# Kernel tuning notes

Measured on AMD Instinct MI355X. Metric: run time of the kernel, lower is better.

The kernel has to match this reference:

```python
import jax, jax.numpy as jnp
import numpy as np

N = 50000
LEAKY_SLOPE = 0.2


def gat_layer(x, src, dst, W, a_src, a_dst, bias, concat):
    """PyG-style GATConv (eval mode, self-loops already in src/dst).
    x: [N, Fin]; W: [Fin, H*C]; a_src, a_dst: [H, C]; bias: [H*C] or [C].
    """
    H, C = a_src.shape
    h = (x @ W).reshape(-1, H, C)                      # [N, H, C]
    alpha_src = jnp.einsum('nhc,hc->nh', h, a_src)      # [N, H]
    alpha_dst = jnp.einsum('nhc,hc->nh', h, a_dst)      # [N, H]
    e = jax.nn.leaky_relu(alpha_src[src] + alpha_dst[dst], LEAKY_SLOPE)  # [E, H]
    # scatter-softmax over incoming edges of each destination node
    m = jax.lax.stop_gradient(jax.ops.segment_max(e, dst, num_segments=N))
    e = jnp.exp(e - m[dst])
    denom = jax.ops.segment_sum(e, dst, num_segments=N)  # [N, H]
    alpha = e / (denom[dst] + 1e-16)                     # [E, H]
    msg = h[src] * alpha[:, :, None]                     # [E, H, C]
    out = jax.ops.segment_sum(msg, dst, num_segments=N)  # [N, H, C]
    out = out.reshape(-1, H * C) if concat else out.mean(axis=1)
    return out + bias


def setup_inputs() -> dict:
    key = jax.random.key(0)
    ks = jax.random.split(key, 10)
    Fin, Hd, Hh = 256, 64, 4
    E = 1600000
    x = jax.random.normal(ks[0], (N, Fin), dtype=jnp.float32)
    edge_index = jax.random.randint(ks[1], (2, E), 0, N, dtype=jnp.int64)
    s = 1.0 / np.sqrt(Fin)
    W1 = jax.random.normal(ks[2], (Fin, Hh * Hd), dtype=jnp.float32) * s
    att_src1 = jax.random.normal(ks[3], (Hh, Hd), dtype=jnp.float32) * (1.0 / np.sqrt(Hd))
    att_dst1 = jax.random.normal(ks[4], (Hh, Hd), dtype=jnp.float32) * (1.0 / np.sqrt(Hd))
    b1 = jnp.zeros((Hh * Hd,), dtype=jnp.float32)
    W2 = jax.random.normal(ks[5], (Hh * Hd, Hd), dtype=jnp.float32) * (1.0 / np.sqrt(Hh * Hd))
    att_src2 = jax.random.normal(ks[6], (1, Hd), dtype=jnp.float32) * (1.0 / np.sqrt(Hd))
    att_dst2 = jax.random.normal(ks[7], (1, Hd), dtype=jnp.float32) * (1.0 / np.sqrt(Hd))
    b2 = jnp.zeros((Hd,), dtype=jnp.float32)
    return {"x": x, "edge_index": edge_index, "W1": W1, "att_src1": att_src1,
            "att_dst1": att_dst1, "b1": b1, "W2": W2, "att_src2": att_src2,
            "att_dst2": att_dst2, "b2": b2}


def reference(x, edge_index, W1, att_src1, att_dst1, b1, W2, att_src2, att_dst2, b2):
    # PyG GATConv adds self-loops by default
    loop = jnp.arange(N, dtype=edge_index.dtype)
    src = jnp.concatenate([edge_index[0], loop])
    dst = jnp.concatenate([edge_index[1], loop])
    h = gat_layer(x, src, dst, W1, att_src1, att_dst1, b1, concat=True)
    h = jax.nn.elu(h)            # dropout is identity in eval mode
    out = gat_layer(h, src, dst, W2, att_src2, att_dst2, b2, concat=False)
    return out
```

## Files before the change

kernel.cpp:

```cpp
#include <hip/hip_runtime.h>


typedef __attribute__((ext_vector_type(8))) short short8;
typedef __attribute__((ext_vector_type(4))) float floatx4;
typedef __attribute__((ext_vector_type(2))) float fx2;
typedef __attribute__((ext_vector_type(4))) unsigned int uintx4;

#define FIN 256
#define H1 4
#define CH 64
#define CAP 16384
#define G2S 40

__device__ __forceinline__ float bf2f(ushort u) {
    union { unsigned int i; float f; } v; v.i = ((unsigned int)u) << 16; return v.f;
}
__device__ __forceinline__ ushort f2bf(float f) {
    union { float f; unsigned int i; } v; v.f = f;
    unsigned int r = v.i + 0x7fffu + ((v.i >> 16) & 1u);
    return (ushort)(r >> 16);
}
__device__ __forceinline__ float load_in(const void* p, int i, int f) {
    return f ? ((const float*)p)[i] : bf2f(((const ushort*)p)[i]);
}
__device__ __forceinline__ int load_idx(const void* p, long long i, int f64) {
    return f64 ? (int)((const long long*)p)[i] : ((const int*)p)[i];
}

__device__ __forceinline__ int pk_off(int row, int k, int KT) {
    return (((row >> 4) * KT + (k >> 5)) << 9) + (((k >> 3) & 3) << 7) +
           ((row & 15) << 3) + (k & 7);
}
__device__ __forceinline__ void pk_dec(int po0, int& row, int& k) {
    int tile = po0 >> 9;
    row = ((tile >> 3) << 4) + ((po0 >> 3) & 15);
    k = ((tile & 7) << 5) + (((po0 >> 7) & 3) << 3);
}

__device__ __forceinline__ float edge_p(float s) {
    s = fmaxf(s, 0.2f * s);
    return __expf(s);
}

__device__ __forceinline__ void accum16(fx2* acc, uint4 v0, uint4 v1,
                                        float p, float& l) {
    l += p;
    fx2 pv = {p, p};
    unsigned w[8] = {v0.x, v0.y, v0.z, v0.w, v1.x, v1.y, v1.z, v1.w};
#pragma unroll
    for (int u = 0; u < 8; ++u) {
        union { unsigned i; float fl; } lo, hi;
        lo.i = w[u] << 16; hi.i = w[u] & 0xffff0000u;
        fx2 c = {lo.fl, hi.fl};
        acc[u] += pv * c;
    }
}

__device__ __forceinline__ void accum8(fx2* acc, uint4 v, float p, float& l) {
    l += p;
    fx2 pv = {p, p};
    unsigned w[4] = {v.x, v.y, v.z, v.w};
#pragma unroll
    for (int u = 0; u < 4; ++u) {
        union { unsigned i; float fl; } lo, hi;
        lo.i = w[u] << 16; hi.i = w[u] & 0xffff0000u;
        fx2 c = {lo.fl, hi.fl};
        acc[u] += pv * c;
    }
}

__global__ __launch_bounds__(256) void probe_kernel(const ushort* __restrict__ x,
                                                    const int* __restrict__ ei,
                                                    int* __restrict__ flags,
                                                    int* __restrict__ bcnt) {
    __shared__ int s_nan, s_odd;
    int t = threadIdx.x;
    bcnt[t] = 0;
    if (t == 0) { s_nan = 0; s_odd = 0; }
    __syncthreads();
    int nanc = 0, oddc = 0;
    for (int i = t; i < 16384; i += 256) {
        ushort u = x[i];
        if (((u >> 7) & 0xFF) == 0xFF) nanc++;
    }
    for (int i = t; i < 2048; i += 256)
        if (ei[2 * i + 1] != 0) oddc++;
    if (nanc) atomicAdd(&s_nan, nanc);
    if (oddc) atomicAdd(&s_odd, oddc);
    __syncthreads();
    if (t == 0) {
        flags[0] = (s_nan >= 2) ? 1 : 0;
        flags[1] = (s_odd == 0) ? 1 : 0;
    }
}

__global__ __launch_bounds__(256) void prep_bucket_kernel(
        const void* __restrict__ x, const void* __restrict__ W1,
        const void* __restrict__ W2, ushort* __restrict__ xb,
        ushort* __restrict__ Wt1, ushort* __restrict__ Wt2,
        const void* __restrict__ ei, int* __restrict__ bcnt,
        unsigned int* __restrict__ buckets,
        int E, int Etot, int Nn, const int* __restrict__ flags,
        int PB_conv, int PB_tr_end) {
    __shared__ int lcnt[256], lbase[256], lcur[256];
    int bid = blockIdx.x, t = threadIdx.x;
    int f = flags[0];
    if (bid < PB_conv) {
        int po0 = bid * 2048 + t * 8;
        int row, k0; pk_dec(po0, row, k0);
        int si = row * FIN + k0;
        if (f) {
            float4 v0 = ((const float4*)x)[si / 4];
            float4 v1 = ((const float4*)x)[si / 4 + 1];
            ushort4 o0, o1;
            o0.x = f2bf(v0.x); o0.y = f2bf(v0.y); o0.z = f2bf(v0.z); o0.w = f2bf(v0.w);
            o1.x = f2bf(v1.x); o1.y = f2bf(v1.y); o1.z = f2bf(v1.z); o1.w = f2bf(v1.w);
            *(ushort4*)(xb + po0) = o0;
            *(ushort4*)(xb + po0 + 4) = o1;
        } else {
            *(uint4*)(xb + po0) = ((const uint4*)x)[si / 8];
        }
        return;
    }
    if (bid < PB_tr_end) {
        int j = (bid - PB_conv) * 256 + t;
        if (j < (FIN * FIN) / 8) {
            int po0 = j * 8;
            int n, k0; pk_dec(po0, n, k0);
            ushort4 o0, o1;
            o0.x = f2bf(load_in(W1, (k0 + 0) * FIN + n, f));
            o0.y = f2bf(load_in(W1, (k0 + 1) * FIN + n, f));
            o0.z = f2bf(load_in(W1, (k0 + 2) * FIN + n, f));
            o0.w = f2bf(load_in(W1, (k0 + 3) * FIN + n, f));
            o1.x = f2bf(load_in(W1, (k0 + 4) * FIN + n, f));
            o1.y = f2bf(load_in(W1, (k0 + 5) * FIN + n, f));
            o1.z = f2bf(load_in(W1, (k0 + 6) * FIN + n, f));
            o1.w = f2bf(load_in(W1, (k0 + 7) * FIN + n, f));
            *(ushort4*)(Wt1 + po0) = o0;
            *(ushort4*)(Wt1 + po0 + 4) = o1;
        } else {
            int po0 = (j - (FIN * FIN) / 8) * 8;
            int n, k0; pk_dec(po0, n, k0);
            ushort4 o0, o1;
            o0.x = f2bf(load_in(W2, (k0 + 0) * CH + n, f));
            o0.y = f2bf(load_in(W2, (k0 + 1) * CH + n, f));
            o0.z = f2bf(load_in(W2, (k0 + 2) * CH + n, f));
            o0.w = f2bf(load_in(W2, (k0 + 3) * CH + n, f));
            o1.x = f2bf(load_in(W2, (k0 + 4) * CH + n, f));
            o1.y = f2bf(load_in(W2, (k0 + 5) * CH + n, f));
            o1.z = f2bf(load_in(W2, (k0 + 6) * CH + n, f));
            o1.w = f2bf(load_in(W2, (k0 + 7) * CH + n, f));
            *(ushort4*)(Wt2 + po0) = o0;
            *(ushort4*)(Wt2 + po0 + 4) = o1;
        }
        return;
    }
    lcnt[t] = 0; lcur[t] = 0;
    __syncthreads();
    int f64 = flags[1];
    int base = (bid - PB_tr_end) * 4096 + t;
    unsigned int val[16]; int bk[16]; bool ok[16];
#pragma unroll
    for (int j = 0; j < 16; ++j) {
        int e = base + j * 256;
        ok[j] = e < Etot;
        bk[j] = 0; val[j] = 0;
        if (ok[j]) {
            int s, d;
            if (e < E) {
                s = load_idx(ei, e, f64);
                d = load_idx(ei, (long long)E + e, f64);
            } else {
                s = d = e - E;
            }
            s = min(max(s, 0), Nn - 1);
            d = min(max(d, 0), Nn - 1);
            bk[j] = d >> 8;
            val[j] = ((unsigned int)s << 8) | (unsigned int)(d & 255);
            atomicAdd(&lcnt[bk[j]], 1);
        }
    }
    __syncthreads();
    if (lcnt[t] > 0) lbase[t] = atomicAdd(&bcnt[t], lcnt[t]);
    __syncthreads();
#pragma unroll
    for (int j = 0; j < 16; ++j) {
        if (ok[j]) {
            int p = lbase[bk[j]] + atomicAdd(&lcur[bk[j]], 1);
            if (p < CAP) buckets[(size_t)bk[j] * CAP + p] = val[j];
        }
    }
}

__device__ __forceinline__ void gemm_core(const ushort* __restrict__ A,
                                          const ushort* __restrict__ Bt,
                                          ushort* __restrict__ C,
                                          int M,
                                          const void* __restrict__ aS,
                                          const void* __restrict__ aD,
                                          float* __restrict__ alphaS,
                                          float* __restrict__ alphaD,
                                          int f, int gx, int head) {
    const int KT = FIN >> 5;
    int tid = threadIdx.x;
    int wave = tid >> 6, lane = tid & 63, quad = lane >> 4, l16 = lane & 15;
    int rbase = gx * 256 + wave * 64;
    int cbase = head * 64;
    int lsub = (quad << 7) + (l16 << 3);
    floatx4 acc[4][4];
#pragma unroll
    for (int i = 0; i < 4; i++)
#pragma unroll
        for (int j = 0; j < 4; j++) acc[i][j] = (floatx4)0.f;

#pragma unroll 2
    for (int kb = 0; kb < FIN; kb += 32) {
        int kt = kb >> 5;
        short8 a[4], b[4];
#pragma unroll
        for (int mt = 0; mt < 4; mt++) {
            int tr = (rbase + mt * 16) >> 4;
            a[mt] = *reinterpret_cast<const short8*>(
                A + (((size_t)(tr * KT + kt)) << 9) + lsub);
        }
#pragma unroll
        for (int nt = 0; nt < 4; nt++) {
            int tc = (cbase + nt * 16) >> 4;
            b[nt] = *reinterpret_cast<const short8*>(
                Bt + (((size_t)(tc * KT + kt)) << 9) + lsub);
        }
#pragma unroll
        for (int mt = 0; mt < 4; mt++)
#pragma unroll
            for (int nt = 0; nt < 4; nt++)
                acc[mt][nt] = __builtin_amdgcn_mfma_f32_16x16x32_bf16(
                    a[mt], b[nt], acc[mt][nt], 0, 0, 0);
    }
    float asv[4], adv[4];
#pragma unroll
    for (int nt = 0; nt < 4; nt++) {
        int col = cbase + nt * 16 + l16;
        asv[nt] = load_in(aS, col, f);
        adv[nt] = load_in(aD, col, f);
    }
#pragma unroll
    for (int mt = 0; mt < 4; mt++) {
#pragma unroll
        for (int r = 0; r < 4; r++) {
            int row = rbase + mt * 16 + quad * 4 + r;
            float ps = 0.f, pd = 0.f;
#pragma unroll
            for (int nt = 0; nt < 4; nt++) {
                float w = acc[mt][nt][r];
                ps += w * asv[nt];
                pd += w * adv[nt];
            }
#pragma unroll
            for (int off = 8; off > 0; off >>= 1) {
                ps += __shfl_xor(ps, off, 16);
                pd += __shfl_xor(pd, off, 16);
            }
            if (row < M) {
                if (l16 == 0) {
                    alphaS[row * H1 + head] = ps;
                    alphaD[row * H1 + head] = pd;
                }
#pragma unroll
                for (int nt = 0; nt < 4; nt++) {
                    int col = cbase + nt * 16 + l16;
                    size_t caddr = ((size_t)(col >> 7) * M + row) * 128 + (col & 127);
                    C[caddr] = f2bf(acc[mt][nt][r]);
                }
            }
        }
    }
}

__global__ __launch_bounds__(256) void gemm1_pass2_kernel(
        const ushort* __restrict__ A, const ushort* __restrict__ Bt,
        ushort* __restrict__ C, int M,
        const void* __restrict__ aS, const void* __restrict__ aD,
        float* __restrict__ alphaS, float* __restrict__ alphaD,
        const int* __restrict__ flags, int NB, int nbx,
        const int* __restrict__ bcnt, const unsigned int* __restrict__ buckets,
        int* __restrict__ offs, int* __restrict__ csr_src, int Nn) {
    __shared__ int part[256], sc[256], sc4[4][256];
    int bid = blockIdx.x;
    int t = threadIdx.x;
    if (bid >= NB) {
        int gg = bid - NB;
        int r = (gg & 7) | ((gg >> 5) << 3);
        int h = (gg >> 3) & 3;
        if (r < nbx)
            gemm_core(A, Bt, C, M, aS, aD, alphaS, alphaD, flags[0], r, h);
        return;
    }
    int b = bid;
    int w = t >> 6;
    part[t] = bcnt[t];
    sc4[0][t] = 0; sc4[1][t] = 0; sc4[2][t] = 0; sc4[3][t] = 0;
    __syncthreads();
#pragma unroll
    for (int off = 1; off < 256; off <<= 1) {
        int v = (t >= off) ? part[t - off] : 0;
        __syncthreads();
        part[t] += v;
        __syncthreads();
    }
    int basepos = (b == 0) ? 0 : part[b - 1];
    int nEdges = min(bcnt[b], CAP);
    const unsigned int* bk = buckets + (size_t)b * CAP;
    for (int i = t; i < nEdges; i += 256)
        atomicAdd(&sc4[w][bk[i] & 255], 1);
    __syncthreads();
    int c0 = sc4[0][t], c1 = sc4[1][t], c2 = sc4[2][t], c3 = sc4[3][t];
    int mycount = c0 + c1 + c2 + c3;
    sc[t] = mycount;
    __syncthreads();
#pragma unroll
    for (int off = 1; off < 256; off <<= 1) {
        int v = (t >= off) ? sc[t - off] : 0;
        __syncthreads();
        sc[t] += v;
        __syncthreads();
    }
    int excl = sc[t] - mycount;
    int gnode = b * 256 + t;
    if (gnode <= Nn) offs[gnode] = basepos + excl;
    sc4[0][t] = excl;
    sc4[1][t] = excl + c0;
    sc4[2][t] = excl + c0 + c1;
    sc4[3][t] = excl + c0 + c1 + c2;
    __syncthreads();
    for (int i = t; i < nEdges; i += 256) {
        unsigned int v = bk[i];
        int p = atomicAdd(&sc4[w][v & 255], 1);
        csr_src[basepos + p] = (int)(v >> 8);
    }
}

__global__ __launch_bounds__(256) void gemm2_kernel(const ushort* __restrict__ A,
                                                    const ushort* __restrict__ Bt,
                                                    ushort* __restrict__ C,
                                                    int M,
                                                    const void* __restrict__ aS,
                                                    const void* __restrict__ aD,
                                                    float* __restrict__ alphaS,
                                                    float* __restrict__ alphaD,
                                                    const int* __restrict__ flags) {
    __shared__ ushort Asub[256 * G2S];
    const int KT = FIN >> 5;
    int t = threadIdx.x;
    int f = flags[0];
    int wave = t >> 6, lane = t & 63, quad = lane >> 4, l16 = lane & 15;
    int rbase = blockIdx.x * 256 + wave * 64;
    int lsub = (quad << 7) + (l16 << 3);
    int chunk = t & 3, rr = t >> 2;
    floatx4 acc[4][4];
#pragma unroll
    for (int i = 0; i < 4; i++)
#pragma unroll
        for (int j = 0; j < 4; j++) acc[i][j] = (floatx4)0.f;

    for (int kb = 0; kb < FIN; kb += 32) {
        __syncthreads();
#pragma unroll
        for (int rd = 0; rd < 4; ++rd) {
            int row = blockIdx.x * 256 + rd * 64 + rr;
            if (row >= M) row = M - 1;
            uint4 v = *(const uint4*)(A + (size_t)row * FIN + kb + chunk * 8);
            *(uint4*)(Asub + (rd * 64 + rr) * G2S + chunk * 8) = v;
        }
        __syncthreads();
        int kt = kb >> 5;
        short8 b[4];
#pragma unroll
        for (int nt = 0; nt < 4; nt++) {
            b[nt] = *reinterpret_cast<const short8*>(
                Bt + (((size_t)(nt * KT + kt)) << 9) + lsub);
        }
#pragma unroll
        for (int mt = 0; mt < 4; mt++) {
            short8 a = *reinterpret_cast<const short8*>(
                Asub + (wave * 64 + mt * 16 + l16) * G2S + quad * 8);
#pragma unroll
            for (int nt = 0; nt < 4; nt++)
                acc[mt][nt] = __builtin_amdgcn_mfma_f32_16x16x32_bf16(
                    a, b[nt], acc[mt][nt], 0, 0, 0);
        }
    }
    float asv[4], adv[4];
#pragma unroll
    for (int nt = 0; nt < 4; nt++) {
        int col = nt * 16 + l16;
        asv[nt] = load_in(aS, col, f);
        adv[nt] = load_in(aD, col, f);
    }
#pragma unroll
    for (int mt = 0; mt < 4; mt++) {
#pragma unroll
        for (int r = 0; r < 4; r++) {
            int row = rbase + mt * 16 + quad * 4 + r;
            float ps = 0.f, pd = 0.f;
#pragma unroll
            for (int nt = 0; nt < 4; nt++) {
                float w = acc[mt][nt][r];
                ps += w * asv[nt];
                pd += w * adv[nt];
            }
#pragma unroll
            for (int off = 8; off > 0; off >>= 1) {
                ps += __shfl_xor(ps, off, 16);
                pd += __shfl_xor(pd, off, 16);
            }
            if (row < M) {
                if (l16 == 0) {
                    alphaS[row] = ps;
                    alphaD[row] = pd;
                }
#pragma unroll
                for (int nt = 0; nt < 4; nt++) {
                    int col = nt * 16 + l16;
                    C[(size_t)row * CH + col] = f2bf(acc[mt][nt][r]);
                }
            }
        }
    }
}

__global__ __launch_bounds__(256) void gat_node1_pass(
        const int* __restrict__ csr_src, const int* __restrict__ offs,
        const float* __restrict__ asrc, const float* __restrict__ adst,
        const ushort* __restrict__ h1p, const void* __restrict__ b1,
        ushort* __restrict__ hmidb, int Nn, const int* __restrict__ flags,
        int plane) {
    int f = flags[0];
    int wave = threadIdx.x >> 6, lane = threadIdx.x & 63;
    int n = blockIdx.x * 4 + wave;
    if (n >= Nn) return;
    int slot = lane >> 3, cg = lane & 7;
    int head = plane * 2 + (cg >> 2);
    float ad = adst[n * H1 + head];
    unsigned rowbase = (unsigned)(plane * Nn) * 128u + (unsigned)cg * 16u;
    int beg = offs[n], end = offs[n + 1];
    fx2 acc[8];
#pragma unroll
    for (int u = 0; u < 8; ++u) acc[u] = (fx2)0.f;
    float l = 0.f;

    int e = beg;
    while (e + 16 <= end) {
        int sa = csr_src[e + slot];
        int sb = csr_src[e + 8 + slot];
        float aa = asrc[sa * H1 + head];
        float ab = asrc[sb * H1 + head];
        const uint4* ra = (const uint4*)(h1p + rowbase + (unsigned)sa * 128u);
        const uint4* rb = (const uint4*)(h1p + rowbase + (unsigned)sb * 128u);
        uint4 va0 = ra[0], va1 = ra[1];
        uint4 vb0 = rb[0], vb1 = rb[1];
        float pa = edge_p(aa + ad);
        float pb = edge_p(ab + ad);
        accum16(acc, va0, va1, pa, l);
        accum16(acc, vb0, vb1, pb, l);
        e += 16;
    }
    if (e < end) {
        int ea = e + slot, eb = e + 8 + slot;
        bool oka = ea < end, okb = eb < end;
        int sa = csr_src[oka ? ea : beg];
        int sb = csr_src[okb ? eb : beg];
        float aa = asrc[sa * H1 + head];
        float ab = asrc[sb * H1 + head];
        const uint4* ra = (const uint4*)(h1p + rowbase + (unsigned)sa * 128u);
        const uint4* rb = (const uint4*)(h1p + rowbase + (unsigned)sb * 128u);
        uint4 va0 = ra[0], va1 = ra[1];
        uint4 vb0 = rb[0], vb1 = rb[1];
        float pa = edge_p(oka ? aa + ad : -1e30f);
        float pb = edge_p(okb ? ab + ad : -1e30f);
        accum16(acc, va0, va1, pa, l);
        accum16(acc, vb0, vb1, pb, l);
    }
#pragma unroll
    for (int off = 8; off <= 32; off <<= 1) {
#pragma unroll
        for (int u = 0; u < 8; ++u) {
            acc[u][0] += __shfl_xor(acc[u][0], off);
            acc[u][1] += __shfl_xor(acc[u][1], off);
        }
        l += __shfl_xor(l, off);
    }
    if (slot == 0) {
        float inv = 1.f / (l + 1e-16f);
        int cb = plane * 128 + cg * 16;
        unsigned ow[8];
#pragma unroll
        for (int u = 0; u < 8; ++u) {
            float o0 = acc[u][0] * inv + load_in(b1, cb + 2 * u, f);
            float o1 = acc[u][1] * inv + load_in(b1, cb + 2 * u + 1, f);
            o0 = o0 > 0.f ? o0 : __expf(o0) - 1.f;
            o1 = o1 > 0.f ? o1 : __expf(o1) - 1.f;
            ow[u] = (unsigned)f2bf(o0) | ((unsigned)f2bf(o1) << 16);
        }
        uintx4 st0 = {ow[0], ow[1], ow[2], ow[3]};
        uintx4 st1 = {ow[4], ow[5], ow[6], ow[7]};
        uintx4* dst = (uintx4*)(hmidb + (size_t)n * 256 + cb);
        __builtin_nontemporal_store(st0, dst);
        __builtin_nontemporal_store(st1, dst + 1);
    }
}

__global__ __launch_bounds__(256) void gat_node2(const int* __restrict__ csr_src,
                                                 const int* __restrict__ offs,
                                                 const float* __restrict__ asrc,
                                                 const float* __restrict__ adst,
                                                 const ushort* __restrict__ h2b,
                                                 const void* __restrict__ b2,
                                                 void* __restrict__ out, int Nn,
                                                 const int* __restrict__ flags) {
    int f = flags[0];
    int wave = threadIdx.x >> 6, lane = threadIdx.x & 63;
    int n = blockIdx.x * 4 + wave;
    if (n >= Nn) return;
    int slot = lane >> 3, cg = lane & 7;
    float ad = adst[n];
    unsigned rowoff = (unsigned)cg * 8u;
    int beg = offs[n], end = offs[n + 1];
    fx2 acc[4];
#pragma unroll
    for (int u = 0; u < 4; ++u) acc[u] = (fx2)0.f;
    float l = 0.f;

    int e = beg;
    while (e + 16 <= end) {
        int sa = csr_src[e + slot];
        int sb = csr_src[e + 8 + slot];
        float aa = asrc[sa];
        float ab = asrc[sb];
        uint4 va = *(const uint4*)(h2b + rowoff + (unsigned)sa * 64u);
        uint4 vb = *(const uint4*)(h2b + rowoff + (unsigned)sb * 64u);
        float pa = edge_p(aa + ad);
        float pb = edge_p(ab + ad);
        accum8(acc, va, pa, l);
        accum8(acc, vb, pb, l);
        e += 16;
    }
    if (e < end) {
        int ea = e + slot, eb = e + 8 + slot;
        bool oka = ea < end, okb = eb < end;
        int sa = csr_src[oka ? ea : beg];
        int sb = csr_src[okb ? eb : beg];
        float aa = asrc[sa];
        float ab = asrc[sb];
        uint4 va = *(const uint4*)(h2b + rowoff + (unsigned)sa * 64u);
        uint4 vb = *(const uint4*)(h2b + rowoff + (unsigned)sb * 64u);
        float pa = edge_p(oka ? aa + ad : -1e30f);
        float pb = edge_p(okb ? ab + ad : -1e30f);
        accum8(acc, va, pa, l);
        accum8(acc, vb, pb, l);
    }
#pragma unroll
    for (int off = 8; off <= 32; off <<= 1) {
#pragma unroll
        for (int u = 0; u < 4; ++u) {
            acc[u][0] += __shfl_xor(acc[u][0], off);
            acc[u][1] += __shfl_xor(acc[u][1], off);
        }
        l += __shfl_xor(l, off);
    }
    if (slot == 0) {
        float inv = 1.f / (l + 1e-16f);
        float o[8];
#pragma unroll
        for (int u = 0; u < 4; ++u) {
            o[2 * u]     = acc[u][0] * inv + load_in(b2, cg * 8 + 2 * u, f);
            o[2 * u + 1] = acc[u][1] * inv + load_in(b2, cg * 8 + 2 * u + 1, f);
        }
        if (f) {
            float* op = (float*)out + (unsigned)n * 64u + (unsigned)cg * 8u;
            floatx4 s0 = {o[0], o[1], o[2], o[3]};
            floatx4 s1 = {o[4], o[5], o[6], o[7]};
            __builtin_nontemporal_store(s0, (floatx4*)op);
            __builtin_nontemporal_store(s1, (floatx4*)(op + 4));
        } else {
            uintx4 st = {(unsigned)f2bf(o[0]) | ((unsigned)f2bf(o[1]) << 16),
                         (unsigned)f2bf(o[2]) | ((unsigned)f2bf(o[3]) << 16),
                         (unsigned)f2bf(o[4]) | ((unsigned)f2bf(o[5]) << 16),
                         (unsigned)f2bf(o[6]) | ((unsigned)f2bf(o[7]) << 16)};
            __builtin_nontemporal_store(st,
                (uintx4*)((ushort*)out + (unsigned)n * 64u + (unsigned)cg * 8u));
        }
    }
}

extern "C" void kernel_launch(void* const* d_in, const int* in_sizes, int n_in,
                              void* d_out, int out_size, void* d_ws, size_t ws_size,
                              hipStream_t stream) {
    const void* x   = d_in[0];
    const void* ei  = d_in[1];
    const void* W1  = d_in[2];
    const void* as1 = d_in[3];
    const void* ad1 = d_in[4];
    const void* b1  = d_in[5];
    const void* W2  = d_in[6];
    const void* as2 = d_in[7];
    const void* ad2 = d_in[8];
    const void* b2  = d_in[9];

    const int Nn = in_sizes[0] / FIN;
    const int E  = in_sizes[1] / 2;
    const int ET = E + Nn;
    const int NB = (Nn + 255) >> 8;

    char* ws = (char*)d_ws;
    size_t off = 0;
    auto alloc = [&](size_t bytes) {
        size_t o = off;
        off += (bytes + 255) & ~(size_t)255;
        return o;
    };
    ushort* xb    = (ushort*)(ws + alloc((size_t)Nn * FIN * 2));
    ushort* h1b   = (ushort*)(ws + alloc((size_t)Nn * FIN * 2));
    ushort* hmidb = (ushort*)(ws + alloc((size_t)Nn * FIN * 2));
    ushort* h2b   = (ushort*)(ws + alloc((size_t)Nn * CH * 2));
    ushort* Wt1   = (ushort*)(ws + alloc((size_t)FIN * FIN * 2));
    ushort* Wt2   = (ushort*)(ws + alloc((size_t)CH * FIN * 2));
    float* as1f   = (float*)(ws + alloc((size_t)Nn * H1 * 4));
    float* ad1f   = (float*)(ws + alloc((size_t)Nn * H1 * 4));
    float* as2f   = (float*)(ws + alloc((size_t)Nn * 4));
    float* ad2f   = (float*)(ws + alloc((size_t)Nn * 4));
    int*   offs   = (int*)(ws + alloc((size_t)(Nn + 1) * 4));
    int*   csr    = (int*)(ws + alloc((size_t)ET * 4));
    unsigned int* buckets = (unsigned int*)(ws + alloc((size_t)256 * CAP * 4));
    int*   bcnt   = (int*)(ws + alloc(256 * 4));
    int*   flags  = (int*)(ws + alloc(256));
    (void)ws_size; (void)n_in; (void)out_size;

    probe_kernel<<<1, 256, 0, stream>>>((const ushort*)x, (const int*)ei, flags, bcnt);

    int PB_conv = (Nn * FIN) / 2048;
    int PB_tr   = (FIN * FIN + CH * FIN) / 2048;
    int PB_bkt  = (ET + 4095) / 4096;
    prep_bucket_kernel<<<PB_conv + PB_tr + PB_bkt, 256, 0, stream>>>(
        x, W1, W2, xb, Wt1, Wt2, ei, bcnt, buckets,
        E, ET, Nn, flags, PB_conv, PB_conv + PB_tr);

    int nbx = (Nn + 255) / 256;
    int ngrp = (nbx + 7) >> 3;
    gemm1_pass2_kernel<<<NB + ngrp * 32, 256, 0, stream>>>(
        xb, Wt1, h1b, Nn, as1, ad1, as1f, ad1f,
        flags, NB, nbx, bcnt, buckets, offs, csr, Nn);

    gat_node1_pass<<<(Nn + 3) / 4, 256, 0, stream>>>(
        csr, offs, as1f, ad1f, h1b, b1, hmidb, Nn, flags, 0);
    gat_node1_pass<<<(Nn + 3) / 4, 256, 0, stream>>>(
        csr, offs, as1f, ad1f, h1b, b1, hmidb, Nn, flags, 1);

    gemm2_kernel<<<(Nn + 255) / 256, 256, 0, stream>>>(
        hmidb, Wt2, h2b, Nn, as2, ad2, as2f, ad2f, flags);
    gat_node2<<<(Nn + 3) / 4, 256, 0, stream>>>(csr, offs, as2f, ad2f, h2b, b2, d_out, Nn, flags);
}
```

Measured before the change: 344.8 us.

## Read raw bf16 input directly in GEMM1 via LDS staging, skip packing copy

When the input is already bf16, the prep kernel no longer repacks x into the MFMA-tiled layout. GEMM1 instead stages row-major tiles of raw x into a padded shared-memory buffer and feeds MFMA from LDS. This removes a full pass over the input array, at the cost of two block barriers per K step and extra LDS in the fused kernel, which may lower occupancy for the bucket/CSR blocks. The probe kernel is also vectorised to uint4 loads.

```diff
diff --git a/kernel.cpp b/kernel.cpp
--- a/kernel.cpp
+++ b/kernel.cpp
@@ -69,8 +69,8 @@
     }
 }
 
-__global__ __launch_bounds__(256) void probe_kernel(const ushort* __restrict__ x,
-                                                    const int* __restrict__ ei,
+__global__ __launch_bounds__(256) void probe_kernel(const uint4* __restrict__ x4,
+                                                    const uint4* __restrict__ ei4,
                                                     int* __restrict__ flags,
                                                     int* __restrict__ bcnt) {
     __shared__ int s_nan, s_odd;
@@ -79,12 +79,22 @@
     if (t == 0) { s_nan = 0; s_odd = 0; }
     __syncthreads();
     int nanc = 0, oddc = 0;
-    for (int i = t; i < 16384; i += 256) {
-        ushort u = x[i];
-        if (((u >> 7) & 0xFF) == 0xFF) nanc++;
-    }
-    for (int i = t; i < 2048; i += 256)
-        if (ei[2 * i + 1] != 0) oddc++;
+#pragma unroll
+    for (int j = 0; j < 4; ++j) {
+        uint4 v = x4[t * 4 + j];
+        unsigned w[4] = {v.x, v.y, v.z, v.w};
+#pragma unroll
+        for (int u = 0; u < 4; ++u) {
+            if (((w[u] >> 7) & 0xFFu) == 0xFFu) nanc++;
+            if (((w[u] >> 23) & 0xFFu) == 0xFFu) nanc++;
+        }
+    }
+#pragma unroll
+    for (int j = 0; j < 4; ++j) {
+        uint4 v = ei4[t * 4 + j];
+        if (v.y != 0u) oddc++;
+        if (v.w != 0u) oddc++;
+    }
     if (nanc) atomicAdd(&s_nan, nanc);
     if (oddc) atomicAdd(&s_odd, oddc);
     __syncthreads();
@@ -106,20 +116,17 @@
     int bid = blockIdx.x, t = threadIdx.x;
     int f = flags[0];
     if (bid < PB_conv) {
+        if (!f) return;
         int po0 = bid * 2048 + t * 8;
         int row, k0; pk_dec(po0, row, k0);
         int si = row * FIN + k0;
-        if (f) {
-            float4 v0 = ((const float4*)x)[si / 4];
-            float4 v1 = ((const float4*)x)[si / 4 + 1];
-            ushort4 o0, o1;
-            o0.x = f2bf(v0.x); o0.y = f2bf(v0.y); o0.z = f2bf(v0.z); o0.w = f2bf(v0.w);
-            o1.x = f2bf(v1.x); o1.y = f2bf(v1.y); o1.z = f2bf(v1.z); o1.w = f2bf(v1.w);
-            *(ushort4*)(xb + po0) = o0;
-            *(ushort4*)(xb + po0 + 4) = o1;
-        } else {
-            *(uint4*)(xb + po0) = ((const uint4*)x)[si / 8];
-        }
+        float4 v0 = ((const float4*)x)[si / 4];
+        float4 v1 = ((const float4*)x)[si / 4 + 1];
+        ushort4 o0, o1;
+        o0.x = f2bf(v0.x); o0.y = f2bf(v0.y); o0.z = f2bf(v0.z); o0.w = f2bf(v0.w);
+        o1.x = f2bf(v1.x); o1.y = f2bf(v1.y); o1.z = f2bf(v1.z); o1.w = f2bf(v1.w);
+        *(ushort4*)(xb + po0) = o0;
+        *(ushort4*)(xb + po0 + 4) = o1;
         return;
     }
     if (bid < PB_tr_end) {
@@ -192,7 +199,9 @@
     }
 }
 
-__device__ __forceinline__ void gemm_core(const ushort* __restrict__ A,
+__device__ __forceinline__ void gemm_core(const ushort* __restrict__ Axb,
+                                          const ushort* __restrict__ Xraw,
+                                          ushort* __restrict__ Asub,
                                           const ushort* __restrict__ Bt,
                                           ushort* __restrict__ C,
                                           int M,
@@ -213,28 +222,60 @@
 #pragma unroll
         for (int j = 0; j < 4; j++) acc[i][j] = (floatx4)0.f;
 
+    if (f) {
 #pragma unroll 2
-    for (int kb = 0; kb < FIN; kb += 32) {
-        int kt = kb >> 5;
-        short8 a[4], b[4];
-#pragma unroll
-        for (int mt = 0; mt < 4; mt++) {
-            int tr = (rbase + mt * 16) >> 4;
-            a[mt] = *reinterpret_cast<const short8*>(
-                A + (((size_t)(tr * KT + kt)) << 9) + lsub);
-        }
-#pragma unroll
-        for (int nt = 0; nt < 4; nt++) {
-            int tc = (cbase + nt * 16) >> 4;
-            b[nt] = *reinterpret_cast<const short8*>(
-                Bt + (((size_t)(tc * KT + kt)) << 9) + lsub);
-        }
-#pragma unroll
-        for (int mt = 0; mt < 4; mt++)
-#pragma unroll
-            for (int nt = 0; nt < 4; nt++)
-                acc[mt][nt] = __builtin_amdgcn_mfma_f32_16x16x32_bf16(
-                    a[mt], b[nt], acc[mt][nt], 0, 0, 0);
+        for (int kb = 0; kb < FIN; kb += 32) {
+            int kt = kb >> 5;
+            short8 a[4], b[4];
+#pragma unroll
+            for (int mt = 0; mt < 4; mt++) {
+                int tr = (rbase + mt * 16) >> 4;
+                a[mt] = *reinterpret_cast<const short8*>(
+                    Axb + (((size_t)(tr * KT + kt)) << 9) + lsub);
+            }
+#pragma unroll
+            for (int nt = 0; nt < 4; nt++) {
+                int tc = (cbase + nt * 16) >> 4;
+                b[nt] = *reinterpret_cast<const short8*>(
+                    Bt + (((size_t)(tc * KT + kt)) << 9) + lsub);
+            }
+#pragma unroll
+            for (int mt = 0; mt < 4; mt++)
+#pragma unroll
+                for (int nt = 0; nt < 4; nt++)
+                    acc[mt][nt] = __builtin_amdgcn_mfma_f32_16x16x32_bf16(
+                        a[mt], b[nt], acc[mt][nt], 0, 0, 0);
+        }
+    } else {
+        int chunk = tid & 3, rr = tid >> 2;
+        for (int kb = 0; kb < FIN; kb += 32) {
+            __syncthreads();
+#pragma unroll
+            for (int rd = 0; rd < 4; ++rd) {
+                int row = gx * 256 + rd * 64 + rr;
+                if (row >= M) row = M - 1;
+                uint4 v = *(const uint4*)(Xraw + (size_t)row * FIN + kb + chunk * 8);
+                *(uint4*)(Asub + (rd * 64 + rr) * G2S + chunk * 8) = v;
+            }
+            __syncthreads();
+            int kt = kb >> 5;
+            short8 b[4];
+#pragma unroll
+            for (int nt = 0; nt < 4; nt++) {
+                int tc = (cbase + nt * 16) >> 4;
+                b[nt] = *reinterpret_cast<const short8*>(
+                    Bt + (((size_t)(tc * KT + kt)) << 9) + lsub);
+            }
+#pragma unroll
+            for (int mt = 0; mt < 4; mt++) {
+                short8 a = *reinterpret_cast<const short8*>(
+                    Asub + (wave * 64 + mt * 16 + l16) * G2S + quad * 8);
+#pragma unroll
+                for (int nt = 0; nt < 4; nt++)
+                    acc[mt][nt] = __builtin_amdgcn_mfma_f32_16x16x32_bf16(
+                        a, b[nt], acc[mt][nt], 0, 0, 0);
+            }
+        }
     }
     float asv[4], adv[4];
 #pragma unroll
@@ -277,7 +318,8 @@
 }
 
 __global__ __launch_bounds__(256) void gemm1_pass2_kernel(
-        const ushort* __restrict__ A, const ushort* __restrict__ Bt,
+        const ushort* __restrict__ Axb, const ushort* __restrict__ Xraw,
+        const ushort* __restrict__ Bt,
         ushort* __restrict__ C, int M,
         const void* __restrict__ aS, const void* __restrict__ aD,
         float* __restrict__ alphaS, float* __restrict__ alphaD,
@@ -285,6 +327,7 @@
         const int* __restrict__ bcnt, const unsigned int* __restrict__ buckets,
         int* __restrict__ offs, int* __restrict__ csr_src, int Nn) {
     __shared__ int part[256], sc[256], sc4[4][256];
+    __shared__ ushort Asub[256 * G2S];
     int bid = blockIdx.x;
     int t = threadIdx.x;
     if (bid >= NB) {
@@ -292,7 +335,8 @@
         int r = (gg & 7) | ((gg >> 5) << 3);
         int h = (gg >> 3) & 3;
         if (r < nbx)
-            gemm_core(A, Bt, C, M, aS, aD, alphaS, alphaD, flags[0], r, h);
+            gemm_core(Axb, Xraw, Asub, Bt, C, M, aS, aD, alphaS, alphaD,
+                      flags[0], r, h);
         return;
     }
     int b = bid;
@@ -635,7 +679,7 @@
     int*   flags  = (int*)(ws + alloc(256));
     (void)ws_size; (void)n_in; (void)out_size;
 
-    probe_kernel<<<1, 256, 0, stream>>>((const ushort*)x, (const int*)ei, flags, bcnt);
+    probe_kernel<<<1, 256, 0, stream>>>((const uint4*)x, (const uint4*)ei, flags, bcnt);
 
     int PB_conv = (Nn * FIN) / 2048;
     int PB_tr   = (FIN * FIN + CH * FIN) / 2048;
@@ -647,7 +691,7 @@
     int nbx = (Nn + 255) / 256;
     int ngrp = (nbx + 7) >> 3;
     gemm1_pass2_kernel<<<NB + ngrp * 32, 256, 0, stream>>>(
-        xb, Wt1, h1b, Nn, as1, ad1, as1f, ad1f,
+        xb, (const ushort*)x, Wt1, h1b, Nn, as1, ad1, as1f, ad1f,
         flags, NB, nbx, bcnt, buckets, offs, csr, Nn);
 
     gat_node1_pass<<<(Nn + 3) / 4, 256, 0, stream>>>(
```

Result: faster. 335.5 us (median of 2 runs) (-2.7%).
